# Performance work log

Measured on AMD Instinct MI355X. Metric: run time of the kernel, lower is better.

The kernel has to match this reference:

```python
import jax, jax.numpy as jnp
import numpy as np

NUM_PITCHES = 88
H_FEAT = 188
LSTM_UNITS = 48
N_STATES = 5
CTX_HID = 16
CTX_OUT = 4


def _glorot(key, shape):
    fan_in, fan_out = shape[1], shape[0]
    lim = (6.0 / (fan_in + fan_out)) ** 0.5
    return jax.random.uniform(key, shape, jnp.float32, -lim, lim)


def setup_inputs() -> dict:
    key = jax.random.key(0)
    ks = jax.random.split(key, 16)
    B, T = 16, 256
    pitch_features = jax.random.normal(ks[0], (B, NUM_PITCHES, H_FEAT, T), jnp.float32)
    prev_context = jax.random.uniform(ks[1], (B, NUM_PITCHES, 3), jnp.float32)
    # context net params
    fc1_w = _glorot(ks[2], (CTX_HID, 3)); fc1_b = jnp.zeros((CTX_HID,), jnp.float32)
    fc2_w = _glorot(ks[3], (CTX_HID, CTX_HID)); fc2_b = jnp.zeros((CTX_HID,), jnp.float32)
    fc3_w = _glorot(ks[4], (CTX_OUT, CTX_HID)); fc3_b = jnp.zeros((CTX_OUT,), jnp.float32)
    # lstm1: input H_FEAT+4 -> 48; gates order i,f,g,o (torch convention)
    in1 = H_FEAT + CTX_OUT
    lstm1_wih = _glorot(ks[5], (4 * LSTM_UNITS, in1))
    lstm1_whh = _glorot(ks[6], (4 * LSTM_UNITS, LSTM_UNITS))
    lstm1_bih = jnp.zeros((4 * LSTM_UNITS,), jnp.float32)
    lstm1_bhh = jnp.zeros((4 * LSTM_UNITS,), jnp.float32)
    lstm2_wih = _glorot(ks[7], (4 * LSTM_UNITS, LSTM_UNITS))
    lstm2_whh = _glorot(ks[8], (4 * LSTM_UNITS, LSTM_UNITS))
    lstm2_bih = jnp.zeros((4 * LSTM_UNITS,), jnp.float32)
    lstm2_bhh = jnp.zeros((4 * LSTM_UNITS,), jnp.float32)
    fc_states_w = _glorot(ks[9], (N_STATES, LSTM_UNITS))
    fc_states_b = jnp.zeros((N_STATES,), jnp.float32)
    return dict(pitch_features=pitch_features, prev_context=prev_context,
                fc1_w=fc1_w, fc1_b=fc1_b, fc2_w=fc2_w, fc2_b=fc2_b,
                fc3_w=fc3_w, fc3_b=fc3_b,
                lstm1_wih=lstm1_wih, lstm1_whh=lstm1_whh, lstm1_bih=lstm1_bih, lstm1_bhh=lstm1_bhh,
                lstm2_wih=lstm2_wih, lstm2_whh=lstm2_whh, lstm2_bih=lstm2_bih, lstm2_bhh=lstm2_bhh,
                fc_states_w=fc_states_w, fc_states_b=fc_states_b)


def _lstm_scan(x, wih, whh, bih, bhh):
    # x: (S, N, In); zero init state; returns (S, N, U)
    S, N, _ = x.shape
    U = whh.shape[1]
    xg = jnp.einsum('sni,gi->sng', x, wih) + bih + bhh  # precompute input gates

    def step(carry, xg_t):
        h, c = carry
        g = xg_t + h @ whh.T  # (N, 4U)
        i, f, gg, o = jnp.split(g, 4, axis=-1)
        c = jax.nn.sigmoid(f) * c + jax.nn.sigmoid(i) * jnp.tanh(gg)
        h = jax.nn.sigmoid(o) * jnp.tanh(c)
        return (h, c), h

    init = (jnp.zeros((N, U), x.dtype), jnp.zeros((N, U), x.dtype))
    _, hs = jax.lax.scan(step, init, xg)
    return hs


def reference(pitch_features, prev_context,
              fc1_w, fc1_b, fc2_w, fc2_b, fc3_w, fc3_b,
              lstm1_wih, lstm1_whh, lstm1_bih, lstm1_bhh,
              lstm2_wih, lstm2_whh, lstm2_bih, lstm2_bhh,
              fc_states_w, fc_states_b):
    B, P, H, T = pitch_features.shape
    # Context net (context never updates across t in the original loop)
    x = jax.nn.relu(prev_context @ fc1_w.T + fc1_b)
    x = jax.nn.relu(x @ fc2_w.T + fc2_b)
    ctx_emb = x @ fc3_w.T + fc3_b  # (B, P, 4)
    # Each timestep t is independent: LSTM runs over the pitch axis (len 88)
    # with zero initial state every step. Fold (B, T) into batch N.
    pf = jnp.transpose(pitch_features, (1, 0, 3, 2)).reshape(P, B * T, H)  # (P, BT, H)
    ce = jnp.broadcast_to(ctx_emb[:, None, :, :], (B, T, P, CTX_OUT))
    ce = jnp.transpose(ce, (2, 0, 1, 3)).reshape(P, B * T, CTX_OUT)
    seq = jnp.concatenate([pf, ce], axis=-1)  # (P, BT, H+4)
    h = _lstm_scan(seq, lstm1_wih, lstm1_whh, lstm1_bih, lstm1_bhh)
    h = _lstm_scan(h, lstm2_wih, lstm2_whh, lstm2_bih, lstm2_bhh)
    logits = h @ fc_states_w.T + fc_states_b  # (P, BT, 5)
    logits = logits.reshape(P, B, T, N_STATES)
    logits = jnp.transpose(logits, (1, 0, 3, 2))  # (B, P, 5, T)
    return jax.nn.softmax(logits, axis=2)
```

## Files before the change

### kernel.cpp

```cpp
#include <hip/hip_runtime.h>
#include <hip/hip_bf16.h>
#include <cstdint>

#define P_ 88
#define B_ 16
#define T_ 256
#define H_ 188
#define G_ 192
#define U_ 48
#define N_ 4096

typedef __attribute__((ext_vector_type(8))) short bf16x8;
typedef __attribute__((ext_vector_type(8))) _Float16 f16x8;
typedef __attribute__((ext_vector_type(4))) float f32x4;

__device__ __forceinline__ float sigf(float x) {
  return __builtin_amdgcn_rcpf(1.0f + __expf(-x));
}
__device__ __forceinline__ float tanh_f(float x) {
  return 1.0f - 2.0f * __builtin_amdgcn_rcpf(1.0f + __expf(2.0f * x));
}
__device__ __forceinline__ unsigned short f2bs(float v) {
  union { __hip_bfloat16 h; unsigned short s; } u;
  u.h = __float2bfloat16(v);
  return u.s;
}
__device__ __forceinline__ float bs2f(unsigned short s) {
  union { unsigned int u; float f; } x;
  x.u = ((unsigned int)s) << 16;
  return x.f;
}
__device__ __forceinline__ float hs2f(unsigned short s) {
  union { unsigned short u; _Float16 h; } x;
  x.u = s;
  return (float)x.h;
}
__device__ __forceinline__ unsigned short f2hs(float v) {
  union { _Float16 h; unsigned short s; } x;
  x.h = (_Float16)v;
  return x.s;
}

__global__ void ctx_kernel(const float* __restrict__ pc,
                           const float* __restrict__ fc1w, const float* __restrict__ fc1b,
                           const float* __restrict__ fc2w, const float* __restrict__ fc2b,
                           const float* __restrict__ fc3w, const float* __restrict__ fc3b,
                           const float* __restrict__ wih1,
                           const float* __restrict__ bih1, const float* __restrict__ bhh1,
                           float* __restrict__ ctxg) {
  int bp = blockIdx.x * 64 + threadIdx.x;
  if (bp >= B_ * P_) return;
  float p0 = pc[bp * 3 + 0], p1 = pc[bp * 3 + 1], p2 = pc[bp * 3 + 2];
  float x1[16], x2[16];
#pragma unroll
  for (int jj = 0; jj < 16; ++jj)
    x1[jj] = fmaxf(0.f, fc1w[jj * 3 + 0] * p0 + fc1w[jj * 3 + 1] * p1 + fc1w[jj * 3 + 2] * p2 + fc1b[jj]);
#pragma unroll
  for (int jj = 0; jj < 16; ++jj) {
    float s = fc2b[jj];
#pragma unroll
    for (int i = 0; i < 16; ++i) s += fc2w[jj * 16 + i] * x1[i];
    x2[jj] = fmaxf(0.f, s);
  }
  float ce[4];
#pragma unroll
  for (int jj = 0; jj < 4; ++jj) {
    float s = fc3b[jj];
#pragma unroll
    for (int i = 0; i < 16; ++i) s += fc3w[jj * 16 + i] * x2[i];
    ce[jj] = s;
  }
  float* op = ctxg + (size_t)bp * G_;
  for (int g = 0; g < G_; ++g) {
    const float* wr = wih1 + (size_t)g * G_ + H_;
    op[g] = bih1[g] + bhh1[g] + ce[0] * wr[0] + ce[1] * wr[1] + ce[2] * wr[2] + ce[3] * wr[3];
  }
}

__global__ __launch_bounds__(256) void wfrag_kernel(const float* __restrict__ wih1,
                                                    f16x8* __restrict__ wfrag) {
  const int idx = blockIdx.x * 256 + threadIdx.x;
  if (idx >= 12 * 6 * 64) return;
  const int l = idx & 63;
  const int kc = (idx >> 6) % 6;
  const int j = idx / 384;
  const int g = j * 16 + (l & 15);
  const int k0 = kc * 32 + (l >> 4) * 8;
  f16x8 v;
#pragma unroll
  for (int e = 0; e < 8; ++e) {
    const int k = k0 + e;
    const float wv = (k < H_) ? wih1[(size_t)g * G_ + k] : 0.f;
    v[e] = (_Float16)wv;
  }
  wfrag[idx] = v;
}

__global__ __launch_bounds__(256, 3) void gemm_mfma(const float* __restrict__ pf,
                                                    const f16x8* __restrict__ wfrag,
                                                    const float* __restrict__ ctxg,
                                                    unsigned short* __restrict__ xg2) {
  const int bp = blockIdx.x >> 1, tb = blockIdx.x & 1;
  const int p = bp % P_, b = bp / P_;
  const int tid = threadIdx.x;
  const int w = tid >> 6, l = tid & 63;
  const int lj = l & 15, lq = l >> 4;

  __shared__ __align__(16) char ldsraw[49152];
  _Float16(*Ahi)[34] = (_Float16(*)[34])ldsraw;
  _Float16(*Alo)[34] = (_Float16(*)[34])(ldsraw + 8704);

  float cg[12];
#pragma unroll
  for (int jn = 0; jn < 12; ++jn)
    cg[jn] = ctxg[(size_t)bp * G_ + jn * 16 + lj];

  f32x4 acc[2][12];
#pragma unroll
  for (int mt = 0; mt < 2; ++mt)
#pragma unroll
    for (int jn = 0; jn < 12; ++jn)
#pragma unroll
      for (int r = 0; r < 4; ++r) acc[mt][jn][r] = 0.f;

  const float* Ab = pf + (size_t)bp * H_ * T_ + tb * 128;
  const int kl = tid >> 5;
  const int t4 = (tid & 31) * 4;

  for (int kc = 0; kc < 6; ++kc) {
    __syncthreads();
#pragma unroll
    for (int rr = 0; rr < 4; ++rr) {
      const int kk = rr * 8 + kl;
      const int kg = kc * 32 + kk;
      float a0 = 0.f, a1 = 0.f, a2 = 0.f, a3 = 0.f;
      if (kg < H_) {
        const float4 v = *(const float4*)(Ab + (size_t)kg * T_ + t4);
        a0 = v.x; a1 = v.y; a2 = v.z; a3 = v.w;
      }
      const _Float16 h0 = (_Float16)a0, h1 = (_Float16)a1;
      const _Float16 h2 = (_Float16)a2, h3 = (_Float16)a3;
      Ahi[t4 + 0][kk] = h0; Alo[t4 + 0][kk] = (_Float16)(a0 - (float)h0);
      Ahi[t4 + 1][kk] = h1; Alo[t4 + 1][kk] = (_Float16)(a1 - (float)h1);
      Ahi[t4 + 2][kk] = h2; Alo[t4 + 2][kk] = (_Float16)(a2 - (float)h2);
      Ahi[t4 + 3][kk] = h3; Alo[t4 + 3][kk] = (_Float16)(a3 - (float)h3);
    }
    __syncthreads();
    const int trow = w * 32;
    const f16x8 ahi0 = *(const f16x8*)&Ahi[trow + lj][lq * 8];
    const f16x8 ahi1 = *(const f16x8*)&Ahi[trow + 16 + lj][lq * 8];
    const f16x8 alo0 = *(const f16x8*)&Alo[trow + lj][lq * 8];
    const f16x8 alo1 = *(const f16x8*)&Alo[trow + 16 + lj][lq * 8];
#pragma unroll
    for (int jn = 0; jn < 12; ++jn) {
      const f16x8 wf = wfrag[(jn * 6 + kc) * 64 + l];
      acc[0][jn] = __builtin_amdgcn_mfma_f32_16x16x32_f16(ahi0, wf, acc[0][jn], 0, 0, 0);
      acc[1][jn] = __builtin_amdgcn_mfma_f32_16x16x32_f16(ahi1, wf, acc[1][jn], 0, 0, 0);
      acc[0][jn] = __builtin_amdgcn_mfma_f32_16x16x32_f16(alo0, wf, acc[0][jn], 0, 0, 0);
      acc[1][jn] = __builtin_amdgcn_mfma_f32_16x16x32_f16(alo1, wf, acc[1][jn], 0, 0, 0);
    }
  }
  __syncthreads();

  unsigned short* Cst = (unsigned short*)ldsraw + w * 6144;
#pragma unroll
  for (int mt = 0; mt < 2; ++mt)
#pragma unroll
    for (int jn = 0; jn < 12; ++jn)
#pragma unroll
      for (int r = 0; r < 4; ++r)
        Cst[mt * 3072 + jn * 256 + r * 64 + l] = f2hs(acc[mt][jn][r] + cg[jn]);
  const int nb0 = b * 16 + tb * 8 + w * 2;
  unsigned short* gb = xg2 + ((size_t)p * 256 + nb0) * 3072;
#pragma unroll
  for (int rr = 0; rr < 12; ++rr) {
    const uint4 v = *(const uint4*)(Cst + rr * 512 + l * 8);
    *(uint4*)(gb + rr * 512 + l * 8) = v;
  }
}

__global__ __launch_bounds__(256, 1) void scan_mfma(
    const unsigned short* __restrict__ xg2,
    const float* __restrict__ whh1, const float* __restrict__ wih2,
    const float* __restrict__ whh2, const float* __restrict__ bih2,
    const float* __restrict__ bhh2, const float* __restrict__ fcw,
    const float* __restrict__ fcb, float* __restrict__ out) {
  __shared__ __align__(16) short hh[16][104];
  __shared__ __align__(16) short hl[16][104];
  __shared__ __align__(16) float gs[16][196];
  __shared__ __align__(16) float h2f[16][52];
  __shared__ __align__(16) float fcws[5 * 48];
  __shared__ float logit_s[5][16];
  __shared__ float prob_s[5][16];

  const int tid = threadIdx.x;
  const int w = tid >> 6;
  const int l = tid & 63;
  const int lj = l & 15;
  const int lq = l >> 4;
  const int n0 = blockIdx.x * 16;
  const int b = n0 >> 8, t0 = n0 & 255;

  bf16x8 b1[3][2];
  bf16x8 b2f[3][3];
  float bias2r[3];
#pragma unroll
  for (int i = 0; i < 3; ++i) {
    const int j = w * 48 + i * 16 + lj;
    bias2r[i] = bih2[j] + bhh2[j];
#pragma unroll
    for (int kc = 0; kc < 2; ++kc)
#pragma unroll
      for (int e = 0; e < 8; ++e) {
        const int u = kc * 32 + lq * 8 + e;
        b1[i][kc][e] = (u < U_) ? (short)f2bs(whh1[j * U_ + u]) : (short)0;
      }
#pragma unroll
    for (int kc = 0; kc < 3; ++kc)
#pragma unroll
      for (int e = 0; e < 8; ++e) {
        const int u = kc * 32 + lq * 8 + e;
        b2f[i][kc][e] = (u < U_) ? (short)f2bs(wih2[j * U_ + u])
                                 : (short)f2bs(whh2[j * U_ + (u - U_)]);
      }
  }

  for (int e = tid; e < 16 * 104 / 2; e += 256) {
    ((unsigned int*)hh)[e] = 0u;
    ((unsigned int*)hl)[e] = 0u;
  }
  for (int e = tid; e < 5 * U_; e += 256) fcws[e] = fcw[e];

  int tn[3], tu[3];
  float c1r[3] = {0.f, 0.f, 0.f}, c2r[3] = {0.f, 0.f, 0.f};
#pragma unroll
  for (int s = 0; s < 3; ++s) {
    const int task = tid + 256 * s;
    tn[s] = task / U_;
    tu[s] = task % U_;
  }
  const bool fcth = tid < 80;
  const int fk = tid >> 4, fn = tid & 15;
  const float fcbr = fcth ? fcb[fk] : 0.f;
  const int sk = (tid - 96) >> 4, sn = (tid - 96) & 15;

  unsigned short xp[12];
  {
    const size_t pb = (size_t)blockIdx.x * 3072;
#pragma unroll
    for (int i = 0; i < 3; ++i)
#pragma unroll
      for (int r = 0; r < 4; ++r)
        xp[i * 4 + r] = xg2[pb + (size_t)((w * 3 + i) * 256 + r * 64 + l)];
  }
  const short* hhrow = &hh[lj][0];
  const short* hlrow = &hl[lj][0];
  __syncthreads();

  for (int p = 0; p < P_; ++p) {
    f32x4 c1f[3];
#pragma unroll
    for (int i = 0; i < 3; ++i)
#pragma unroll
      for (int r = 0; r < 4; ++r) c1f[i][r] = hs2f(xp[i * 4 + r]);
    {
      bf16x8 ah0 = *(const bf16x8*)(hhrow + lq * 8);
      bf16x8 ah1 = *(const bf16x8*)(hhrow + 32 + lq * 8);
      bf16x8 al0 = *(const bf16x8*)(hlrow + lq * 8);
      bf16x8 al1 = *(const bf16x8*)(hlrow + 32 + lq * 8);
#pragma unroll
      for (int i = 0; i < 3; ++i)
        c1f[i] = __builtin_amdgcn_mfma_f32_16x16x32_bf16(ah0, b1[i][0], c1f[i], 0, 0, 0);
#pragma unroll
      for (int i = 0; i < 3; ++i)
        c1f[i] = __builtin_amdgcn_mfma_f32_16x16x32_bf16(ah1, b1[i][1], c1f[i], 0, 0, 0);
#pragma unroll
      for (int i = 0; i < 3; ++i)
        c1f[i] = __builtin_amdgcn_mfma_f32_16x16x32_bf16(al0, b1[i][0], c1f[i], 0, 0, 0);
#pragma unroll
      for (int i = 0; i < 3; ++i)
        c1f[i] = __builtin_amdgcn_mfma_f32_16x16x32_bf16(al1, b1[i][1], c1f[i], 0, 0, 0);
    }
#pragma unroll
    for (int i = 0; i < 3; ++i)
#pragma unroll
      for (int r = 0; r < 4; ++r)
        gs[lq * 4 + r][w * 48 + i * 16 + lj] = c1f[i][r];
    if (p > 0 && fcth) {
      float a = fcbr;
#pragma unroll
      for (int uq = 0; uq < 12; ++uq) {
        f32x4 hv = *(const f32x4*)&h2f[fn][uq * 4];
        f32x4 wv = *(const f32x4*)&fcws[fk * 48 + uq * 4];
        a += hv[0] * wv[0] + hv[1] * wv[1] + hv[2] * wv[2] + hv[3] * wv[3];
      }
      logit_s[fk][fn] = a;
    }
    __syncthreads();
#pragma unroll
    for (int s = 0; s < 3; ++s) {
      const int n = tn[s], u = tu[s];
      const float ig = gs[n][u], fg = gs[n][48 + u];
      const float gg = gs[n][96 + u], og = gs[n][144 + u];
      const float cc = sigf(fg) * c1r[s] + sigf(ig) * tanh_f(gg);
      c1r[s] = cc;
      const float h = sigf(og) * tanh_f(cc);
      const unsigned short hb = f2bs(h);
      hh[n][u] = (short)hb;
      hl[n][u] = (short)f2bs(h - bs2f(hb));
    }
    if (p > 0 && tid >= 192 && tid < 208) {
      const int n = tid - 192;
      const float l0 = logit_s[0][n], l1 = logit_s[1][n], l2 = logit_s[2][n],
                  l3 = logit_s[3][n], l4 = logit_s[4][n];
      const float m = fmaxf(fmaxf(fmaxf(l0, l1), fmaxf(l2, l3)), l4);
      const float e0 = __expf(l0 - m), e1 = __expf(l1 - m), e2 = __expf(l2 - m),
                  e3 = __expf(l3 - m), e4 = __expf(l4 - m);
      const float rs = __builtin_amdgcn_rcpf(e0 + e1 + e2 + e3 + e4);
      prob_s[0][n] = e0 * rs; prob_s[1][n] = e1 * rs; prob_s[2][n] = e2 * rs;
      prob_s[3][n] = e3 * rs; prob_s[4][n] = e4 * rs;
    }
    __syncthreads();
    if (p < P_ - 1) {
      const size_t pb = (size_t)((p + 1) * 256 + blockIdx.x) * 3072;
#pragma unroll
      for (int i = 0; i < 3; ++i)
#pragma unroll
        for (int r = 0; r < 4; ++r)
          xp[i * 4 + r] = xg2[pb + (size_t)((w * 3 + i) * 256 + r * 64 + l)];
    }
    f32x4 c2f[3];
#pragma unroll
    for (int i = 0; i < 3; ++i) {
      c2f[i][0] = bias2r[i]; c2f[i][1] = bias2r[i];
      c2f[i][2] = bias2r[i]; c2f[i][3] = bias2r[i];
    }
    {
      bf16x8 a0 = *(const bf16x8*)(hhrow + lq * 8);
      bf16x8 a1 = *(const bf16x8*)(hhrow + 32 + lq * 8);
      bf16x8 a2 = *(const bf16x8*)(hhrow + 64 + lq * 8);
      bf16x8 q0 = *(const bf16x8*)(hlrow + lq * 8);
      bf16x8 q1 = *(const bf16x8*)(hlrow + 32 + lq * 8);
      bf16x8 q2 = *(const bf16x8*)(hlrow + 64 + lq * 8);
#pragma unroll
      for (int i = 0; i < 3; ++i)
        c2f[i] = __builtin_amdgcn_mfma_f32_16x16x32_bf16(a0, b2f[i][0], c2f[i], 0, 0, 0);
#pragma unroll
      for (int i = 0; i < 3; ++i)
        c2f[i] = __builtin_amdgcn_mfma_f32_16x16x32_bf16(a1, b2f[i][1], c2f[i], 0, 0, 0);
#pragma unroll
      for (int i = 0; i < 3; ++i)
        c2f[i] = __builtin_amdgcn_mfma_f32_16x16x32_bf16(a2, b2f[i][2], c2f[i], 0, 0, 0);
#pragma unroll
      for (int i = 0; i < 3; ++i)
        c2f[i] = __builtin_amdgcn_mfma_f32_16x16x32_bf16(q0, b2f[i][0], c2f[i], 0, 0, 0);
#pragma unroll
      for (int i = 0; i < 3; ++i)
        c2f[i] = __builtin_amdgcn_mfma_f32_16x16x32_bf16(q1, b2f[i][1], c2f[i], 0, 0, 0);
#pragma unroll
      for (int i = 0; i < 3; ++i)
        c2f[i] = __builtin_amdgcn_mfma_f32_16x16x32_bf16(q2, b2f[i][2], c2f[i], 0, 0, 0);
    }
#pragma unroll
    for (int i = 0; i < 3; ++i)
#pragma unroll
      for (int r = 0; r < 4; ++r)
        gs[lq * 4 + r][w * 48 + i * 16 + lj] = c2f[i][r];
    if (p > 0 && tid >= 96 && tid < 176) {
      out[(((size_t)b * P_ + (p - 1)) * 5 + sk) * T_ + t0 + sn] = prob_s[sk][sn];
    }
    __syncthreads();
#pragma unroll
    for (int s = 0; s < 3; ++s) {
      const int n = tn[s], u = tu[s];
      const float ig = gs[n][u], fg = gs[n][48 + u];
      const float gg = gs[n][96 + u], og = gs[n][144 + u];
      const float cc = sigf(fg) * c2r[s] + sigf(ig) * tanh_f(gg);
      c2r[s] = cc;
      const float h = sigf(og) * tanh_f(cc);
      const unsigned short hb = f2bs(h);
      hh[n][48 + u] = (short)hb;
      hl[n][48 + u] = (short)f2bs(h - bs2f(hb));
      h2f[n][u] = h;
    }
    __syncthreads();
  }
  if (fcth) {
    float a = fcbr;
#pragma unroll
    for (int uq = 0; uq < 12; ++uq) {
      f32x4 hv = *(const f32x4*)&h2f[fn][uq * 4];
      f32x4 wv = *(const f32x4*)&fcws[fk * 48 + uq * 4];
      a += hv[0] * wv[0] + hv[1] * wv[1] + hv[2] * wv[2] + hv[3] * wv[3];
    }
    logit_s[fk][fn] = a;
  }
  __syncthreads();
  if (tid >= 192 && tid < 208) {
    const int n = tid - 192;
    const float l0 = logit_s[0][n], l1 = logit_s[1][n], l2 = logit_s[2][n],
                l3 = logit_s[3][n], l4 = logit_s[4][n];
    const float m = fmaxf(fmaxf(fmaxf(l0, l1), fmaxf(l2, l3)), l4);
    const float e0 = __expf(l0 - m), e1 = __expf(l1 - m), e2 = __expf(l2 - m),
                e3 = __expf(l3 - m), e4 = __expf(l4 - m);
    const float rs = __builtin_amdgcn_rcpf(e0 + e1 + e2 + e3 + e4);
    prob_s[0][n] = e0 * rs; prob_s[1][n] = e1 * rs; prob_s[2][n] = e2 * rs;
    prob_s[3][n] = e3 * rs; prob_s[4][n] = e4 * rs;
  }
  __syncthreads();
  if (tid >= 96 && tid < 176) {
    out[(((size_t)b * P_ + (P_ - 1)) * 5 + sk) * T_ + t0 + sn] = prob_s[sk][sn];
  }
}

extern "C" void kernel_launch(void* const* d_in, const int* in_sizes, int n_in,
                              void* d_out, int out_size, void* d_ws, size_t ws_size,
                              hipStream_t stream) {
  const float* pf   = (const float*)d_in[0];
  const float* pc   = (const float*)d_in[1];
  const float* fc1w = (const float*)d_in[2];
  const float* fc1b = (const float*)d_in[3];
  const float* fc2w = (const float*)d_in[4];
  const float* fc2b = (const float*)d_in[5];
  const float* fc3w = (const float*)d_in[6];
  const float* fc3b = (const float*)d_in[7];
  const float* wih1 = (const float*)d_in[8];
  const float* whh1 = (const float*)d_in[9];
  const float* bih1 = (const float*)d_in[10];
  const float* bhh1 = (const float*)d_in[11];
  const float* wih2 = (const float*)d_in[12];
  const float* whh2 = (const float*)d_in[13];
  const float* bih2 = (const float*)d_in[14];
  const float* bhh2 = (const float*)d_in[15];
  const float* fcw  = (const float*)d_in[16];
  const float* fcb  = (const float*)d_in[17];
  float* out = (float*)d_out;

  char* wsp = (char*)d_ws;
  float* ctxg = (float*)wsp;
  const size_t CTXG_BYTES = (size_t)B_ * P_ * G_ * sizeof(float);
  f16x8* wfrag = (f16x8*)(wsp + CTXG_BYTES);
  const size_t WFRAG_BYTES = (size_t)12 * 6 * 64 * 16;
  unsigned short* xg2 = (unsigned short*)(wsp + CTXG_BYTES + WFRAG_BYTES);

  ctx_kernel<<<22, 64, 0, stream>>>(pc, fc1w, fc1b, fc2w, fc2b, fc3w, fc3b,
                                    wih1, bih1, bhh1, ctxg);
  wfrag_kernel<<<18, 256, 0, stream>>>(wih1, wfrag);
  gemm_mfma<<<B_ * P_ * 2, 256, 0, stream>>>(pf, wfrag, ctxg, xg2);
  scan_mfma<<<N_ / 16, 256, 0, stream>>>(xg2, whh1, wih2, whh2,
                                         bih2, bhh2, fcw, fcb, out);
}
```

Baseline: 420.9 us.

## Split scan blocks into 8-sequence halves for two blocks per CU

The recurrent scan kernel now gives each block 8 sequences instead of 16, so the grid doubles to 512 blocks, and launch bounds allow two blocks per CU. MFMA tiles stay 16 rows wide, with the upper 8 rows zero-padded. Per-thread elementwise gate work drops from three tasks to at most two. The aim is to hide the latency of the serial 88-step chain and its barriers by interleaving two independent blocks per CU. The cost is doubled MFMA issue per useful row and wasted padding lanes.

Measured after the change: 426.2 us. Within noise of the previous version (+1.3%).

```diff
diff --git a/kernel.cpp b/kernel.cpp
--- a/kernel.cpp
+++ b/kernel.cpp
@@ -179,7 +179,7 @@
   }
 }
 
-__global__ __launch_bounds__(256, 1) void scan_mfma(
+__global__ __launch_bounds__(256, 2) void scan_mfma(
     const unsigned short* __restrict__ xg2,
     const float* __restrict__ whh1, const float* __restrict__ wih2,
     const float* __restrict__ whh2, const float* __restrict__ bih2,
@@ -187,18 +187,20 @@
     const float* __restrict__ fcb, float* __restrict__ out) {
   __shared__ __align__(16) short hh[16][104];
   __shared__ __align__(16) short hl[16][104];
-  __shared__ __align__(16) float gs[16][196];
-  __shared__ __align__(16) float h2f[16][52];
+  __shared__ __align__(16) float gs[8][196];
+  __shared__ __align__(16) float h2f[8][52];
   __shared__ __align__(16) float fcws[5 * 48];
-  __shared__ float logit_s[5][16];
-  __shared__ float prob_s[5][16];
+  __shared__ float logit_s[5][8];
+  __shared__ float prob_s[5][8];
 
   const int tid = threadIdx.x;
   const int w = tid >> 6;
   const int l = tid & 63;
   const int lj = l & 15;
   const int lq = l >> 4;
-  const int n0 = blockIdx.x * 16;
+  const int grp = blockIdx.x >> 1;
+  const int half = blockIdx.x & 1;
+  const int n0 = blockIdx.x * 8;
   const int b = n0 >> 8, t0 = n0 & 255;
 
   bf16x8 b1[3][2];
@@ -231,27 +233,24 @@
   }
   for (int e = tid; e < 5 * U_; e += 256) fcws[e] = fcw[e];
 
-  int tn[3], tu[3];
-  float c1r[3] = {0.f, 0.f, 0.f}, c2r[3] = {0.f, 0.f, 0.f};
-#pragma unroll
-  for (int s = 0; s < 3; ++s) {
-    const int task = tid + 256 * s;
-    tn[s] = task / U_;
-    tu[s] = task % U_;
-  }
-  const bool fcth = tid < 80;
-  const int fk = tid >> 4, fn = tid & 15;
+  const int tn0 = tid / U_, tu0 = tid % U_;
+  const int tn1 = (256 + tid) / U_, tu1 = (256 + tid) % U_;
+  float c1r[2] = {0.f, 0.f}, c2r[2] = {0.f, 0.f};
+  const bool fcth = tid < 40;
+  const int fk = tid >> 3, fn = tid & 7;
   const float fcbr = fcth ? fcb[fk] : 0.f;
-  const int sk = (tid - 96) >> 4, sn = (tid - 96) & 15;
+  const int sk = (tid - 96) >> 3, sn = (tid - 96) & 7;
 
   unsigned short xp[12];
   {
-    const size_t pb = (size_t)blockIdx.x * 3072;
+    const size_t pb = (size_t)grp * 3072;
 #pragma unroll
     for (int i = 0; i < 3; ++i)
 #pragma unroll
       for (int r = 0; r < 4; ++r)
-        xp[i * 4 + r] = xg2[pb + (size_t)((w * 3 + i) * 256 + r * 64 + l)];
+        xp[i * 4 + r] = (lq < 2)
+            ? xg2[pb + (size_t)((w * 3 + i) * 256 + r * 64 + (half * 2 + lq) * 16 + lj)]
+            : (unsigned short)0;
   }
   const short* hhrow = &hh[lj][0];
   const short* hlrow = &hl[lj][0];
@@ -281,11 +280,13 @@
       for (int i = 0; i < 3; ++i)
         c1f[i] = __builtin_amdgcn_mfma_f32_16x16x32_bf16(al1, b1[i][1], c1f[i], 0, 0, 0);
     }
-#pragma unroll
-    for (int i = 0; i < 3; ++i)
-#pragma unroll
-      for (int r = 0; r < 4; ++r)
-        gs[lq * 4 + r][w * 48 + i * 16 + lj] = c1f[i][r];
+    if (lq < 2) {
+#pragma unroll
+      for (int i = 0; i < 3; ++i)
+#pragma unroll
+        for (int r = 0; r < 4; ++r)
+          gs[lq * 4 + r][w * 48 + i * 16 + lj] = c1f[i][r];
+    }
     if (p > 0 && fcth) {
       float a = fcbr;
 #pragma unroll
@@ -297,19 +298,29 @@
       logit_s[fk][fn] = a;
     }
     __syncthreads();
-#pragma unroll
-    for (int s = 0; s < 3; ++s) {
-      const int n = tn[s], u = tu[s];
+    {
+      const int n = tn0, u = tu0;
       const float ig = gs[n][u], fg = gs[n][48 + u];
       const float gg = gs[n][96 + u], og = gs[n][144 + u];
-      const float cc = sigf(fg) * c1r[s] + sigf(ig) * tanh_f(gg);
-      c1r[s] = cc;
+      const float cc = sigf(fg) * c1r[0] + sigf(ig) * tanh_f(gg);
+      c1r[0] = cc;
       const float h = sigf(og) * tanh_f(cc);
       const unsigned short hb = f2bs(h);
       hh[n][u] = (short)hb;
       hl[n][u] = (short)f2bs(h - bs2f(hb));
     }
-    if (p > 0 && tid >= 192 && tid < 208) {
+    if (tid < 128) {
+      const int n = tn1, u = tu1;
+      const float ig = gs[n][u], fg = gs[n][48 + u];
+      const float gg = gs[n][96 + u], og = gs[n][144 + u];
+      const float cc = sigf(fg) * c1r[1] + sigf(ig) * tanh_f(gg);
+      c1r[1] = cc;
+      const float h = sigf(og) * tanh_f(cc);
+      const unsigned short hb = f2bs(h);
+      hh[n][u] = (short)hb;
+      hl[n][u] = (short)f2bs(h - bs2f(hb));
+    }
+    if (p > 0 && tid >= 192 && tid < 200) {
       const int n = tid - 192;
       const float l0 = logit_s[0][n], l1 = logit_s[1][n], l2 = logit_s[2][n],
                   l3 = logit_s[3][n], l4 = logit_s[4][n];
@@ -322,12 +333,14 @@
     }
     __syncthreads();
     if (p < P_ - 1) {
-      const size_t pb = (size_t)((p + 1) * 256 + blockIdx.x) * 3072;
+      const size_t pb = (size_t)((p + 1) * 256 + grp) * 3072;
 #pragma unroll
       for (int i = 0; i < 3; ++i)
 #pragma unroll
         for (int r = 0; r < 4; ++r)
-          xp[i * 4 + r] = xg2[pb + (size_t)((w * 3 + i) * 256 + r * 64 + l)];
+          xp[i * 4 + r] = (lq < 2)
+              ? xg2[pb + (size_t)((w * 3 + i) * 256 + r * 64 + (half * 2 + lq) * 16 + lj)]
+              : (unsigned short)0;
     }
     f32x4 c2f[3];
 #pragma unroll
@@ -361,28 +374,41 @@
       for (int i = 0; i < 3; ++i)
         c2f[i] = __builtin_amdgcn_mfma_f32_16x16x32_bf16(q2, b2f[i][2], c2f[i], 0, 0, 0);
     }
-#pragma unroll
-    for (int i = 0; i < 3; ++i)
-#pragma unroll
-      for (int r = 0; r < 4; ++r)
-        gs[lq * 4 + r][w * 48 + i * 16 + lj] = c2f[i][r];
-    if (p > 0 && tid >= 96 && tid < 176) {
+    if (lq < 2) {
+#pragma unroll
+      for (int i = 0; i < 3; ++i)
+#pragma unroll
+        for (int r = 0; r < 4; ++r)
+          gs[lq * 4 + r][w * 48 + i * 16 + lj] = c2f[i][r];
+    }
+    if (p > 0 && tid >= 96 && tid < 136) {
       out[(((size_t)b * P_ + (p - 1)) * 5 + sk) * T_ + t0 + sn] = prob_s[sk][sn];
     }
     __syncthreads();
-#pragma unroll
-    for (int s = 0; s < 3; ++s) {
-      const int n = tn[s], u = tu[s];
+    {
+      const int n = tn0, u = tu0;
       const float ig = gs[n][u], fg = gs[n][48 + u];
       const float gg = gs[n][96 + u], og = gs[n][144 + u];
-      const float cc = sigf(fg) * c2r[s] + sigf(ig) * tanh_f(gg);
-      c2r[s] = cc;
+      const float cc = sigf(fg) * c2r[0] + sigf(ig) * tanh_f(gg);
+      c2r[0] = cc;
       const float h = sigf(og) * tanh_f(cc);
       const unsigned short hb = f2bs(h);
       hh[n][48 + u] = (short)hb;
       hl[n][48 + u] = (short)f2bs(h - bs2f(hb));
       h2f[n][u] = h;
     }
+    if (tid < 128) {
+      const int n = tn1, u = tu1;
+      const float ig = gs[n][u], fg = gs[n][48 + u];
+      const float gg = gs[n][96 + u], og = gs[n][144 + u];
+      const float cc = sigf(fg) * c2r[1] + sigf(ig) * tanh_f(gg);
+      c2r[1] = cc;
+      const float h = sigf(og) * tanh_f(cc);
+      const unsigned short hb = f2bs(h);
+      hh[n][48 + u] = (short)hb;
+      hl[n][48 + u] = (short)f2bs(h - bs2f(hb));
+      h2f[n][u] = h;
+    }
     __syncthreads();
   }
   if (fcth) {
@@ -396,7 +422,7 @@
     logit_s[fk][fn] = a;
   }
   __syncthreads();
-  if (tid >= 192 && tid < 208) {
+  if (tid >= 192 && tid < 200) {
     const int n = tid - 192;
     const float l0 = logit_s[0][n], l1 = logit_s[1][n], l2 = logit_s[2][n],
                 l3 = logit_s[3][n], l4 = logit_s[4][n];
@@ -408,7 +434,7 @@
     prob_s[3][n] = e3 * rs; prob_s[4][n] = e4 * rs;
   }
   __syncthreads();
-  if (tid >= 96 && tid < 176) {
+  if (tid >= 96 && tid < 136) {
     out[(((size_t)b * P_ + (P_ - 1)) * 5 + sk) * T_ + t0 + sn] = prob_s[sk][sn];
   }
 }
@@ -447,6 +473,6 @@
                                     wih1, bih1, bhh1, ctxg);
   wfrag_kernel<<<18, 256, 0, stream>>>(wih1, wfrag);
   gemm_mfma<<<B_ * P_ * 2, 256, 0, stream>>>(pf, wfrag, ctxg, xg2);
-  scan_mfma<<<N_ / 16, 256, 0, stream>>>(xg2, whh1, wih2, whh2,
-                                         bih2, bhh2, fcw, fcb, out);
-}
+  scan_mfma<<<N_ / 8, 256, 0, stream>>>(xg2, whh1, wih2, whh2,
+                                        bih2, bhh2, fcw, fcb, out);
+}
```
